# Kernel tuning notes

Measured on AMD Instinct MI355X. Metric: run time of the kernel, lower is better.

## Reference

```python
import jax, jax.numpy as jnp
import numpy as np

H = 16           # num_heads
D = 1024         # hidden_size
HD = D // H      # head_dim = 64
LN_EPS = 1e-5


def setup_inputs() -> dict:
    key = jax.random.key(0)
    ks = jax.random.split(key, 11)
    s = 1.0 / np.sqrt(D)
    x = jax.random.normal(ks[0], (2, 2048, D), dtype=jnp.float32)
    Wq = jax.random.uniform(ks[1], (D, D), jnp.float32, -s, s)
    bq = jax.random.uniform(ks[2], (D,), jnp.float32, -s, s)
    Wk = jax.random.uniform(ks[3], (D, D), jnp.float32, -s, s)
    bk = jax.random.uniform(ks[4], (D,), jnp.float32, -s, s)
    Wv = jax.random.uniform(ks[5], (D, D), jnp.float32, -s, s)
    bv = jax.random.uniform(ks[6], (D,), jnp.float32, -s, s)
    Wo = jax.random.uniform(ks[7], (D, D), jnp.float32, -s, s)
    bo = jax.random.uniform(ks[8], (D,), jnp.float32, -s, s)
    gamma = jnp.ones((D,), jnp.float32)
    beta = jnp.zeros((D,), jnp.float32)
    return {"x": x, "Wq": Wq, "bq": bq, "Wk": Wk, "bk": bk,
            "Wv": Wv, "bv": bv, "Wo": Wo, "bo": bo,
            "gamma": gamma, "beta": beta}


def reference(x, Wq, bq, Wk, bk, Wv, bv, Wo, bo, gamma, beta):
    B, S, _ = x.shape
    # projections -> [B, H, S, HD]
    def split_heads(t):
        return t.reshape(B, S, H, HD).transpose(0, 2, 1, 3)
    Q = split_heads(x @ Wq + bq)
    K = split_heads(x @ Wk + bk)
    V = split_heads(x @ Wv + bv)
    # scores [B, H, S, S], softmax over keys (dropout = identity in eval)
    scores = jnp.einsum('bhqd,bhkd->bhqk', Q, K) / np.sqrt(HD).astype(np.float32)
    attn = jax.nn.softmax(scores, axis=-1)
    ctx = jnp.einsum('bhqk,bhkd->bhqd', attn, V)          # [B, H, S, HD]
    ctx = ctx.transpose(0, 2, 1, 3).reshape(B, S, H * HD)  # [B, S, D]
    out = ctx @ Wo + bo
    # residual + LayerNorm
    y = out + x
    mu = jnp.mean(y, axis=-1, keepdims=True)
    var = jnp.mean(jnp.square(y - mu), axis=-1, keepdims=True)
    return (y - mu) * jax.lax.rsqrt(var + LN_EPS) * gamma + beta
```

## Files before the change

kernel.cpp:

```cpp
#include <hip/hip_runtime.h>
#include <cstdint>
#include <cstddef>


typedef short  b16x8  __attribute__((ext_vector_type(8)));
typedef float  f32x4  __attribute__((ext_vector_type(4)));
typedef float  f32x16 __attribute__((ext_vector_type(16)));

#define AS1 __attribute__((address_space(1)))
#define AS3 __attribute__((address_space(3)))

__device__ __forceinline__ unsigned short f2bf(float f) {
    unsigned int u = __builtin_bit_cast(unsigned int, f);
    u += 0x7FFFu + ((u >> 16) & 1u);
    return (unsigned short)(u >> 16);
}

__device__ __forceinline__ unsigned int cvt_pk_bf16(float lo, float hi) {
    unsigned int r;
    asm("v_cvt_pk_bf16_f32 %0, %1, %2" : "=v"(r) : "v"(lo), "v"(hi));
    return r;
}

__device__ __forceinline__ float exp2_fast(float x) {
    float r;
    asm("v_exp_f32 %0, %1" : "=v"(r) : "v"(x));
    return r;
}

__device__ __forceinline__ void permswap(unsigned &a, unsigned &b) {
    asm volatile("v_permlane32_swap_b32 %0, %1" : "+v"(a), "+v"(b));
}

__global__ __launch_bounds__(256) void k_cvt_x(const float* __restrict__ x,
                                               unsigned short* __restrict__ xb) {
    int i = blockIdx.x * 256 + threadIdx.x;
    size_t base = (size_t)i * 8;
    float4 v0 = *(const float4*)(x + base);
    float4 v1 = *(const float4*)(x + base + 4);
    int row = (int)(base >> 10), col = (int)(base & 1023);
    int rt = row >> 7, rr = row & 127, kt = col >> 6, cc = col & 63;
    int e = (rr * 64 + cc) ^ ((rr & 7) << 3);
    unsigned short o[8];
    o[0] = f2bf(v0.x); o[1] = f2bf(v0.y); o[2] = f2bf(v0.z); o[3] = f2bf(v0.w);
    o[4] = f2bf(v1.x); o[5] = f2bf(v1.y); o[6] = f2bf(v1.z); o[7] = f2bf(v1.w);
    *(uint4*)(xb + (size_t)(rt * 16 + kt) * 8192 + e) = *(uint4*)o;
}

__global__ __launch_bounds__(1024) void k_cvt_w(
    const float* __restrict__ W0, const float* __restrict__ W1,
    const float* __restrict__ W2, const float* __restrict__ W3,
    unsigned short* __restrict__ T0, unsigned short* __restrict__ T1,
    unsigned short* __restrict__ T2, unsigned short* __restrict__ T3) {
    const float* W = blockIdx.z == 0 ? W0 : blockIdx.z == 1 ? W1 : blockIdx.z == 2 ? W2 : W3;
    unsigned short* T = blockIdx.z == 0 ? T0 : blockIdx.z == 1 ? T1 : blockIdx.z == 2 ? T2 : T3;
    __shared__ float tile[32][33];
    int k0 = blockIdx.x * 32, n0 = blockIdx.y * 32;
    int tx = threadIdx.x, ty = threadIdx.y;
    tile[ty][tx] = W[(size_t)(k0 + ty) * 1024 + n0 + tx];
    __syncthreads();
    int n = n0 + ty, k = k0 + tx;
    unsigned short v = f2bf(tile[tx][ty]);
    if (blockIdx.z == 3) {
        T[(size_t)n * 1024 + k] = v;
    } else {
        int r = n & 127, c = k & 63;
        int e = (r * 64 + c) ^ ((r & 7) << 3);
        T[(size_t)((n >> 7) * 16 + (k >> 6)) * 8192 + e] = v;
    }
}

__global__ __launch_bounds__(512) void k_gemm_qkv(
    const unsigned short* __restrict__ A, const unsigned short* __restrict__ Bt,
    const float* __restrict__ bq, const float* __restrict__ bk, const float* __restrict__ bv,
    unsigned short* __restrict__ Qb, unsigned short* __restrict__ Kt,
    unsigned short* __restrict__ Vt) {
    __shared__ unsigned short As[2][8192];
    __shared__ unsigned short Bs[2][8192];
    const int tid = threadIdx.x, lane = tid & 63, wid = tid >> 6;
    const int m0 = blockIdx.y * 128, n0 = blockIdx.x * 128;
    const int wr = wid >> 2, wc = wid & 3;
    const int g = lane >> 4, r = lane & 15;
    f32x4 acc[4][2] = {};

    const unsigned short* Abase = A  + (size_t)blockIdx.y * 16 * 8192;
    const unsigned short* Bbase = Bt + (size_t)blockIdx.x * 16 * 8192;

#define GSTAGE(kt, buf) do {                                                              \
        const unsigned short* _a = Abase + (size_t)(kt) * 8192 + tid * 8;                 \
        const unsigned short* _b = Bbase + (size_t)(kt) * 8192 + tid * 8;                 \
        __builtin_amdgcn_global_load_lds((const AS1 void*)(_a),        (AS3 void*)((char*)As[buf] + tid * 16),        16, 0, 0); \
        __builtin_amdgcn_global_load_lds((const AS1 void*)(_a + 4096), (AS3 void*)((char*)As[buf] + 8192 + tid * 16), 16, 0, 0); \
        __builtin_amdgcn_global_load_lds((const AS1 void*)(_b),        (AS3 void*)((char*)Bs[buf] + tid * 16),        16, 0, 0); \
        __builtin_amdgcn_global_load_lds((const AS1 void*)(_b + 4096), (AS3 void*)((char*)Bs[buf] + 8192 + tid * 16), 16, 0, 0); \
    } while (0)

    GSTAGE(0, 0);
    __syncthreads();

    for (int kt = 0; kt < 16; ++kt) {
        const int cur = kt & 1;
        const unsigned short* Ac = As[cur];
        const unsigned short* Bc = Bs[cur];
        if (kt < 15) GSTAGE(kt + 1, cur ^ 1);
#pragma unroll
        for (int kk = 0; kk < 2; ++kk) {
            b16x8 af[4], bfr[2];
#pragma unroll
            for (int mi = 0; mi < 4; ++mi) {
                int row = wr * 64 + mi * 16 + r;
                int e = (row * 64 + kk * 32 + g * 8) ^ ((row & 7) << 3);
                af[mi] = __builtin_bit_cast(b16x8, *(const uint4*)(Ac + e));
            }
#pragma unroll
            for (int ni = 0; ni < 2; ++ni) {
                int row = wc * 32 + ni * 16 + r;
                int e = (row * 64 + kk * 32 + g * 8) ^ ((row & 7) << 3);
                bfr[ni] = __builtin_bit_cast(b16x8, *(const uint4*)(Bc + e));
            }
#pragma unroll
            for (int mi = 0; mi < 4; ++mi)
#pragma unroll
                for (int ni = 0; ni < 2; ++ni)
                    acc[mi][ni] = __builtin_amdgcn_mfma_f32_16x16x32_bf16(af[mi], bfr[ni], acc[mi][ni], 0, 0, 0);
        }
        __syncthreads();
    }
#undef GSTAGE

    for (int ni = 0; ni < 2; ++ni) {
        int col = n0 + wc * 32 + ni * 16 + r;
        int which = col >> 10, c = col & 1023;
        const float* bp = which == 0 ? bq : which == 1 ? bk : bv;
        float bvv = bp[c];
        int h = c >> 6, hd = c & 63;
        for (int mi = 0; mi < 4; ++mi)
            for (int j = 0; j < 4; ++j) {
                int row = m0 + wr * 64 + mi * 16 + g * 4 + j;
                float v = acc[mi][ni][j] + bvv;
                int b = row >> 11, s = row & 2047;
                size_t bh = (size_t)(b * 16 + h);
                if (which == 0) {
                    Qb[(bh * 2048 + s) * 64 + hd] = f2bf(v * 0.180336881f);
                } else if (which == 1) {
                    int tt = s >> 6, kr = s & 63;
                    Kt[(bh * 32 + tt) * 4096 + ((kr * 64 + hd) ^ ((kr & 7) << 3))] = f2bf(v);
                } else {
                    int tt = s >> 6, cc = s & 63;
                    Vt[(bh * 32 + tt) * 4096 + ((hd * 64 + cc) ^ ((hd & 7) << 3))] = f2bf(v);
                }
            }
    }
}

__global__ __launch_bounds__(512) void k_gemm_proj(
    const unsigned short* __restrict__ A, const unsigned short* __restrict__ Bt,
    const float* __restrict__ bias, float* __restrict__ out) {
    __shared__ unsigned short As[2][128 * 32];
    __shared__ unsigned short Bs[2][64 * 32];
    const int tid = threadIdx.x, lane = tid & 63, wid = tid >> 6;
    const int m0 = blockIdx.y * 128, n0 = blockIdx.x * 64;
    const int wr = wid >> 1, wc = wid & 1;
    f32x4 acc[2][2] = {};

    const int srow = tid >> 2, scol = (tid & 3) * 8;
    const unsigned short* Ag = A  + (size_t)(m0 + srow) * 1024 + scol;
    const unsigned short* Bg = Bt + (size_t)(n0 + srow) * 1024 + scol;

#define PSTAGE(kt, buf) do {                                                              \
        __builtin_amdgcn_global_load_lds((const AS1 void*)(Ag + (kt) * 32),               \
                                         (AS3 void*)((char*)As[buf] + tid * 16), 16, 0, 0); \
        if (tid < 256)                                                                    \
            __builtin_amdgcn_global_load_lds((const AS1 void*)(Bg + (kt) * 32),           \
                                             (AS3 void*)((char*)Bs[buf] + tid * 16), 16, 0, 0); \
    } while (0)

    PSTAGE(0, 0);
    __syncthreads();

    const int g = lane >> 4, r = lane & 15;
    for (int kt = 0; kt < 32; ++kt) {
        const int cur = kt & 1;
        if (kt < 31) PSTAGE(kt + 1, cur ^ 1);
        b16x8 af[2], bfr[2];
#pragma unroll
        for (int mi = 0; mi < 2; ++mi)
            af[mi] = __builtin_bit_cast(b16x8, *(const uint4*)(As[cur] + (wr * 32 + mi * 16 + r) * 32 + g * 8));
#pragma unroll
        for (int ni = 0; ni < 2; ++ni)
            bfr[ni] = __builtin_bit_cast(b16x8, *(const uint4*)(Bs[cur] + (wc * 32 + ni * 16 + r) * 32 + g * 8));
#pragma unroll
        for (int mi = 0; mi < 2; ++mi)
#pragma unroll
            for (int ni = 0; ni < 2; ++ni)
                acc[mi][ni] = __builtin_amdgcn_mfma_f32_16x16x32_bf16(af[mi], bfr[ni], acc[mi][ni], 0, 0, 0);
        __syncthreads();
    }
#undef PSTAGE

    for (int mi = 0; mi < 2; ++mi)
        for (int ni = 0; ni < 2; ++ni) {
            int col = n0 + wc * 32 + ni * 16 + r;
            float bv = bias[col];
            for (int j = 0; j < 4; ++j) {
                int row = m0 + wr * 32 + mi * 16 + g * 4 + j;
                out[(size_t)row * 1024 + col] = acc[mi][ni][j] + bv;
            }
        }
}

#define TSWZ(row, byteoff) ((((row) * 128) + (byteoff)) ^ (((row) & 7) << 4))

__global__ __launch_bounds__(512, 4) void k_attn(const unsigned short* __restrict__ Qb,
                                                 const unsigned short* __restrict__ Kt,
                                                 const unsigned short* __restrict__ Vt,
                                                 unsigned short* __restrict__ ctx) {
    __shared__ unsigned short Ks[2][2][4096];
    __shared__ unsigned short Vs[2][2][4096];
    __shared__ float lsh[4][64];
    const int tid = threadIdx.x, lane = tid & 63, w = tid >> 6;
    const int q32 = lane & 31, hi = lane >> 5;
    const int wq = w & 3, grp = w >> 2;
    const int lt = wq * 64 + lane;

    int bid = blockIdx.x;
    int xcd = bid & 7, idx = bid >> 3;
    int bh = xcd * 4 + (idx & 3);
    int q0 = (idx >> 2) * 128;
    const int b = bh >> 4, h = bh & 15;

    const unsigned short* qrow = Qb + ((size_t)bh * 2048 + q0 + wq * 32 + q32) * 64 + hi * 8;
    b16x8 qf[4];
#pragma unroll
    for (int ds = 0; ds < 4; ++ds)
        qf[ds] = __builtin_bit_cast(b16x8, *(const uint4*)(qrow + ds * 16));

    const unsigned short* Kg = Kt + (size_t)bh * 32 * 4096;
    const unsigned short* Vg = Vt + (size_t)bh * 32 * 4096;
    const int ktbase = grp * 16;

#define STAGE(i, buf) do {                                                                \
        const unsigned short* _ks = Kg + (size_t)(ktbase + (i)) * 4096 + lt * 8;          \
        const unsigned short* _vs = Vg + (size_t)(ktbase + (i)) * 4096 + lt * 8;          \
        __builtin_amdgcn_global_load_lds((const AS1 void*)_ks,          (AS3 void*)((char*)Ks[grp][buf] + lt * 16),        16, 0, 0); \
        __builtin_amdgcn_global_load_lds((const AS1 void*)(_ks + 2048), (AS3 void*)((char*)Ks[grp][buf] + 4096 + lt * 16), 16, 0, 0); \
        __builtin_amdgcn_global_load_lds((const AS1 void*)_vs,          (AS3 void*)((char*)Vs[grp][buf] + lt * 16),        16, 0, 0); \
        __builtin_amdgcn_global_load_lds((const AS1 void*)(_vs + 2048), (AS3 void*)((char*)Vs[grp][buf] + 4096 + lt * 16), 16, 0, 0); \
    } while (0)

    float lpart = 0.f;
    f32x16 oacc[2] = {};

    STAGE(0, 0);
    __syncthreads();

    for (int i = 0; i < 16; ++i) {
        const int cur = i & 1;
        if (i < 15) STAGE(i + 1, cur ^ 1);

        f32x16 sacc[2] = {};
        __builtin_amdgcn_s_setprio(1);
#pragma unroll
        for (int ds = 0; ds < 4; ++ds) {
            b16x8 kf0 = __builtin_bit_cast(b16x8, *(const uint4*)((char*)Ks[grp][cur] + TSWZ(q32,      ds * 32 + hi * 16)));
            b16x8 kf1 = __builtin_bit_cast(b16x8, *(const uint4*)((char*)Ks[grp][cur] + TSWZ(32 + q32, ds * 32 + hi * 16)));
            sacc[0] = __builtin_amdgcn_mfma_f32_32x32x16_bf16(kf0, qf[ds], sacc[0], 0, 0, 0);
            sacc[1] = __builtin_amdgcn_mfma_f32_32x32x16_bf16(kf1, qf[ds], sacc[1], 0, 0, 0);
        }
        __builtin_amdgcn_s_setprio(0);

        float pb[2][16];
#pragma unroll
        for (int kb = 0; kb < 2; ++kb)
#pragma unroll
            for (int reg = 0; reg < 16; ++reg)
                pb[kb][reg] = exp2_fast(sacc[kb][reg]);
        {
            float t0 = (pb[0][0]  + pb[0][1])  + (pb[0][2]  + pb[0][3]);
            float t1 = (pb[0][4]  + pb[0][5])  + (pb[0][6]  + pb[0][7]);
            float t2 = (pb[0][8]  + pb[0][9])  + (pb[0][10] + pb[0][11]);
            float t3 = (pb[0][12] + pb[0][13]) + (pb[0][14] + pb[0][15]);
            float t4 = (pb[1][0]  + pb[1][1])  + (pb[1][2]  + pb[1][3]);
            float t5 = (pb[1][4]  + pb[1][5])  + (pb[1][6]  + pb[1][7]);
            float t6 = (pb[1][8]  + pb[1][9])  + (pb[1][10] + pb[1][11]);
            float t7 = (pb[1][12] + pb[1][13]) + (pb[1][14] + pb[1][15]);
            lpart += ((t0 + t1) + (t2 + t3)) + ((t4 + t5) + (t6 + t7));
        }
        unsigned wv[2][4][2];
#pragma unroll
        for (int kb = 0; kb < 2; ++kb)
#pragma unroll
            for (int rg = 0; rg < 4; ++rg) {
                wv[kb][rg][0] = cvt_pk_bf16(pb[kb][rg * 4 + 0], pb[kb][rg * 4 + 1]);
                wv[kb][rg][1] = cvt_pk_bf16(pb[kb][rg * 4 + 2], pb[kb][rg * 4 + 3]);
            }
        b16x8 pa[4];
#pragma unroll
        for (int ks = 0; ks < 4; ++ks) {
            int kb = ks >> 1, rg0 = (ks & 1) * 2;
            unsigned u0 = wv[kb][rg0][0], u2 = wv[kb][rg0 + 1][0];
            permswap(u0, u2);
            unsigned u1 = wv[kb][rg0][1], u3 = wv[kb][rg0 + 1][1];
            permswap(u1, u3);
            uint4 uu; uu.x = u0; uu.y = u1; uu.z = u2; uu.w = u3;
            pa[ks] = __builtin_bit_cast(b16x8, uu);
        }
        __builtin_amdgcn_s_setprio(1);
#pragma unroll
        for (int ks = 0; ks < 4; ++ks) {
            b16x8 vf0 = __builtin_bit_cast(b16x8, *(const uint4*)((char*)Vs[grp][cur] + TSWZ(q32,      ks * 32 + hi * 16)));
            b16x8 vf1 = __builtin_bit_cast(b16x8, *(const uint4*)((char*)Vs[grp][cur] + TSWZ(32 + q32, ks * 32 + hi * 16)));
            oacc[0] = __builtin_amdgcn_mfma_f32_32x32x16_bf16(pa[ks], vf0, oacc[0], 0, 0, 0);
            oacc[1] = __builtin_amdgcn_mfma_f32_32x32x16_bf16(pa[ks], vf1, oacc[1], 0, 0, 0);
        }
        __builtin_amdgcn_s_setprio(0);
        __syncthreads();
    }

    {
        unsigned a = __builtin_bit_cast(unsigned, lpart), bb = a;
        permswap(a, bb);
        lpart = __builtin_bit_cast(float, a) + __builtin_bit_cast(float, bb);
    }

    float* s0 = (float*)Ks[1];
    float* s1 = (float*)Vs[1];
    if (grp == 1) {
        int base = (wq * 64 + lane) * 16;
#pragma unroll
        for (int reg = 0; reg < 16; ++reg) {
            s0[base + reg] = oacc[0][reg];
            s1[base + reg] = oacc[1][reg];
        }
        lsh[wq][lane] = lpart;
    }
    __syncthreads();
    if (grp == 0) {
        float l = lpart + lsh[wq][lane];
        float inv = 1.f / l;
        int base = (wq * 64 + lane) * 16;
#pragma unroll
        for (int reg = 0; reg < 16; ++reg) {
            int qr = (reg & 3) + 8 * (reg >> 2) + 4 * hi;
            float iv = __shfl(inv, qr, 64);
            float o0 = (oacc[0][reg] + s0[base + reg]) * iv;
            float o1 = (oacc[1][reg] + s1[base + reg]) * iv;
            unsigned short* dst = ctx + ((size_t)(b * 2048 + q0 + wq * 32 + qr)) * 1024 + h * 64 + q32;
            dst[0]  = f2bf(o0);
            dst[32] = f2bf(o1);
        }
    }
#undef STAGE
}

__global__ __launch_bounds__(256) void k_ln(const float* __restrict__ proj,
                                            const float* __restrict__ x,
                                            const float* __restrict__ gamma,
                                            const float* __restrict__ beta,
                                            float* __restrict__ out) {
    int t = threadIdx.x, lane = t & 63, w = t >> 6;
    int row = blockIdx.x * 4 + w;
    const float4* pr = (const float4*)(proj + (size_t)row * 1024);
    const float4* xr = (const float4*)(x    + (size_t)row * 1024);
    float4 y[4];
    float s = 0.f, ss = 0.f;
#pragma unroll
    for (int i = 0; i < 4; ++i) {
        float4 a = pr[lane + i * 64], bx = xr[lane + i * 64];
        float4 yy;
        yy.x = a.x + bx.x; yy.y = a.y + bx.y; yy.z = a.z + bx.z; yy.w = a.w + bx.w;
        y[i] = yy;
        s  += yy.x + yy.y + yy.z + yy.w;
        ss += yy.x * yy.x + yy.y * yy.y + yy.z * yy.z + yy.w * yy.w;
    }
#pragma unroll
    for (int o = 32; o > 0; o >>= 1) {
        s  += __shfl_xor(s,  o, 64);
        ss += __shfl_xor(ss, o, 64);
    }
    float mu  = s * (1.f / 1024.f);
    float var = ss * (1.f / 1024.f) - mu * mu;
    float inv = rsqrtf(var + 1e-5f);
    float4* outr = (float4*)(out + (size_t)row * 1024);
    const float4* gr = (const float4*)gamma;
    const float4* br = (const float4*)beta;
#pragma unroll
    for (int i = 0; i < 4; ++i) {
        float4 g4 = gr[lane + i * 64], b4 = br[lane + i * 64];
        float4 o4;
        o4.x = (y[i].x - mu) * inv * g4.x + b4.x;
        o4.y = (y[i].y - mu) * inv * g4.y + b4.y;
        o4.z = (y[i].z - mu) * inv * g4.z + b4.z;
        o4.w = (y[i].w - mu) * inv * g4.w + b4.w;
        outr[lane + i * 64] = o4;
    }
}

extern "C" void kernel_launch(void* const* d_in, const int* in_sizes, int n_in,
                              void* d_out, int out_size, void* d_ws, size_t ws_size,
                              hipStream_t stream) {
    const float* x  = (const float*)d_in[0];
    const float* Wq = (const float*)d_in[1];
    const float* bq = (const float*)d_in[2];
    const float* Wk = (const float*)d_in[3];
    const float* bk = (const float*)d_in[4];
    const float* Wv = (const float*)d_in[5];
    const float* bv = (const float*)d_in[6];
    const float* Wo = (const float*)d_in[7];
    const float* bo = (const float*)d_in[8];
    const float* gamma = (const float*)d_in[9];
    const float* beta  = (const float*)d_in[10];

    char* ws = (char*)d_ws;
    const size_t MB = 1u << 20;
    unsigned short* xbf   = (unsigned short*)(ws);
    unsigned short* Wqkvt = (unsigned short*)(ws + 8 * MB);
    unsigned short* Wot   = (unsigned short*)(ws + 14 * MB);
    unsigned short* Qb    = (unsigned short*)(ws + 16 * MB);
    unsigned short* Kt    = (unsigned short*)(ws + 24 * MB);
    unsigned short* Vt    = (unsigned short*)(ws + 32 * MB);
    float* proj = (float*)(ws + 16 * MB);
    unsigned short* ctx = xbf;

    k_cvt_x<<<2048, 256, 0, stream>>>(x, xbf);
    k_cvt_w<<<dim3(32, 32, 4), dim3(32, 32), 0, stream>>>(
        Wq, Wk, Wv, Wo, Wqkvt, Wqkvt + 1024 * 1024, Wqkvt + 2 * 1024 * 1024, Wot);
    k_gemm_qkv<<<dim3(24, 32), 512, 0, stream>>>(xbf, Wqkvt, bq, bk, bv, Qb, Kt, Vt);
    k_attn<<<512, 512, 0, stream>>>(Qb, Kt, Vt, ctx);
    k_gemm_proj<<<dim3(16, 32), 512, 0, stream>>>(ctx, Wot, bo, proj);
    k_ln<<<1024, 256, 0, stream>>>(proj, x, gamma, beta, (float*)d_out);
}
```

Before: 130.3 us.

## Restructure QKV GEMM into 256x256 tiles with phased prefetch and XCD remap

The QKV projection GEMM moves from 128x128 tiles to 256x256 tiles per 512-thread block. Operands are re-laid out by the conversion kernels into 64-row swizzled sub-tiles and loaded in four phases, with partial vmcnt waits so that loading the next k-step overlaps MFMA work. The 1D grid is remapped so neighbouring tiles land on the same XCD. The goal is more data reuse per LDS byte and less exposed load latency, at the cost of only 192 blocks, which may leave some CUs idle. Separately, the s_setprio hints around the attention MFMA loops are removed.

```diff
diff --git a/kernel.cpp b/kernel.cpp
--- a/kernel.cpp
+++ b/kernel.cpp
@@ -39,12 +39,12 @@
     float4 v0 = *(const float4*)(x + base);
     float4 v1 = *(const float4*)(x + base + 4);
     int row = (int)(base >> 10), col = (int)(base & 1023);
-    int rt = row >> 7, rr = row & 127, kt = col >> 6, cc = col & 63;
+    int qi = row >> 6, rr = row & 63, kt = col >> 6, cc = col & 63;
     int e = (rr * 64 + cc) ^ ((rr & 7) << 3);
     unsigned short o[8];
     o[0] = f2bf(v0.x); o[1] = f2bf(v0.y); o[2] = f2bf(v0.z); o[3] = f2bf(v0.w);
     o[4] = f2bf(v1.x); o[5] = f2bf(v1.y); o[6] = f2bf(v1.z); o[7] = f2bf(v1.w);
-    *(uint4*)(xb + (size_t)(rt * 16 + kt) * 8192 + e) = *(uint4*)o;
+    *(uint4*)(xb + (size_t)(qi * 16 + kt) * 4096 + e) = *(uint4*)o;
 }
 
 __global__ __launch_bounds__(1024) void k_cvt_w(
@@ -64,9 +64,9 @@
     if (blockIdx.z == 3) {
         T[(size_t)n * 1024 + k] = v;
     } else {
-        int r = n & 127, c = k & 63;
-        int e = (r * 64 + c) ^ ((r & 7) << 3);
-        T[(size_t)((n >> 7) * 16 + (k >> 6)) * 8192 + e] = v;
+        int rr = n & 63, cc = k & 63;
+        int e = (rr * 64 + cc) ^ ((rr & 7) << 3);
+        T[(size_t)((n >> 6) * 16 + (k >> 6)) * 4096 + e] = v;
     }
 }
 
@@ -75,69 +75,102 @@
     const float* __restrict__ bq, const float* __restrict__ bk, const float* __restrict__ bv,
     unsigned short* __restrict__ Qb, unsigned short* __restrict__ Kt,
     unsigned short* __restrict__ Vt) {
-    __shared__ unsigned short As[2][8192];
-    __shared__ unsigned short Bs[2][8192];
+    __shared__ unsigned short As[2][4][4096];
+    __shared__ unsigned short Bs[2][4][4096];
     const int tid = threadIdx.x, lane = tid & 63, wid = tid >> 6;
-    const int m0 = blockIdx.y * 128, n0 = blockIdx.x * 128;
     const int wr = wid >> 2, wc = wid & 3;
     const int g = lane >> 4, r = lane & 15;
-    f32x4 acc[4][2] = {};
-
-    const unsigned short* Abase = A  + (size_t)blockIdx.y * 16 * 8192;
-    const unsigned short* Bbase = Bt + (size_t)blockIdx.x * 16 * 8192;
-
-#define GSTAGE(kt, buf) do {                                                              \
-        const unsigned short* _a = Abase + (size_t)(kt) * 8192 + tid * 8;                 \
-        const unsigned short* _b = Bbase + (size_t)(kt) * 8192 + tid * 8;                 \
-        __builtin_amdgcn_global_load_lds((const AS1 void*)(_a),        (AS3 void*)((char*)As[buf] + tid * 16),        16, 0, 0); \
-        __builtin_amdgcn_global_load_lds((const AS1 void*)(_a + 4096), (AS3 void*)((char*)As[buf] + 8192 + tid * 16), 16, 0, 0); \
-        __builtin_amdgcn_global_load_lds((const AS1 void*)(_b),        (AS3 void*)((char*)Bs[buf] + tid * 16),        16, 0, 0); \
-        __builtin_amdgcn_global_load_lds((const AS1 void*)(_b + 4096), (AS3 void*)((char*)Bs[buf] + 8192 + tid * 16), 16, 0, 0); \
-    } while (0)
-
-    GSTAGE(0, 0);
-    __syncthreads();
+
+    int bid = blockIdx.x;
+    int wg = (bid & 7) * 24 + (bid >> 3);
+    int bx = wg % 12, by = wg / 12;
+
+    f32x4 acc[8][4] = {};
+    b16x8 bfr[4][2];
+
+    const unsigned short* Ab = A  + (size_t)(by * 4) * 16 * 4096;
+    const unsigned short* Bb = Bt + (size_t)(bx * 4) * 16 * 4096;
+
+#define SA(kt_, q_, d_) __builtin_amdgcn_global_load_lds(                                  \
+        (const AS1 void*)(Ab + ((size_t)(q_) * 16 + (kt_)) * 4096 + tid * 8),              \
+        (AS3 void*)((char*)As[d_][q_] + tid * 16), 16, 0, 0)
+#define SB(kt_, q_, d_) __builtin_amdgcn_global_load_lds(                                  \
+        (const AS1 void*)(Bb + ((size_t)(q_) * 16 + (kt_)) * 4096 + tid * 8),              \
+        (AS3 void*)((char*)Bs[d_][q_] + tid * 16), 16, 0, 0)
+
+#define LD8(base_, row_, kk_) __builtin_bit_cast(b16x8, *(const uint4*)(                   \
+        (const char*)(base_) + (row_) * 128 + ((((kk_) * 64) + g * 16) ^ (((row_) & 7) << 4))))
+
+#define MFMA16(a_, b_, c_) __builtin_amdgcn_mfma_f32_16x16x32_bf16(a_, b_, c_, 0, 0, 0)
+
+    SA(0, 0, 0); SA(0, 1, 0); SA(0, 2, 0); SA(0, 3, 0);
+    SB(0, 0, 0); SB(0, 1, 0); SB(0, 2, 0); SB(0, 3, 0);
+    SA(1, 0, 1); SA(1, 1, 1);
+
+#define DO_PHASE(p, STAGES)                                                                \
+    {                                                                                      \
+        STAGES                                                                             \
+        if ((p) == 0) {                                                                    \
+            if (kt < 15) asm volatile("s_waitcnt vmcnt(6)" ::: "memory");                  \
+            else         asm volatile("s_waitcnt vmcnt(0)" ::: "memory");                  \
+        }                                                                                  \
+        __builtin_amdgcn_s_barrier();                                                      \
+        __builtin_amdgcn_sched_barrier(0);                                                 \
+        const char* _aq = (const char*)As[d][wr * 2 + ((p) >> 1)];                         \
+        const int _row0 = ((2 * (p)) & 3) * 16 + r;                                        \
+        const int _row1 = ((2 * (p) + 1) & 3) * 16 + r;                                    \
+        b16x8 a0k0 = LD8(_aq, _row0, 0), a0k1 = LD8(_aq, _row0, 1);                        \
+        b16x8 a1k0 = LD8(_aq, _row1, 0), a1k1 = LD8(_aq, _row1, 1);                        \
+        if ((p) == 0) {                                                                    \
+            const char* _bq = (const char*)Bs[d][wc];                                      \
+            _Pragma("unroll")                                                              \
+            for (int ni = 0; ni < 4; ++ni) {                                               \
+                int rowb = ni * 16 + r;                                                    \
+                bfr[ni][0] = LD8(_bq, rowb, 0);                                            \
+                bfr[ni][1] = LD8(_bq, rowb, 1);                                            \
+            }                                                                              \
+        }                                                                                  \
+        __builtin_amdgcn_s_setprio(1);                                                     \
+        _Pragma("unroll")                                                                  \
+        for (int ni = 0; ni < 4; ++ni) {                                                   \
+            acc[2 * (p)][ni]     = MFMA16(a0k0, bfr[ni][0], acc[2 * (p)][ni]);             \
+            acc[2 * (p)][ni]     = MFMA16(a0k1, bfr[ni][1], acc[2 * (p)][ni]);             \
+            acc[2 * (p) + 1][ni] = MFMA16(a1k0, bfr[ni][0], acc[2 * (p) + 1][ni]);         \
+            acc[2 * (p) + 1][ni] = MFMA16(a1k1, bfr[ni][1], acc[2 * (p) + 1][ni]);         \
+        }                                                                                  \
+        __builtin_amdgcn_s_setprio(0);                                                     \
+        __builtin_amdgcn_s_barrier();                                                      \
+        __builtin_amdgcn_sched_barrier(0);                                                 \
+    }
 
     for (int kt = 0; kt < 16; ++kt) {
-        const int cur = kt & 1;
-        const unsigned short* Ac = As[cur];
-        const unsigned short* Bc = Bs[cur];
-        if (kt < 15) GSTAGE(kt + 1, cur ^ 1);
-#pragma unroll
-        for (int kk = 0; kk < 2; ++kk) {
-            b16x8 af[4], bfr[2];
-#pragma unroll
-            for (int mi = 0; mi < 4; ++mi) {
-                int row = wr * 64 + mi * 16 + r;
-                int e = (row * 64 + kk * 32 + g * 8) ^ ((row & 7) << 3);
-                af[mi] = __builtin_bit_cast(b16x8, *(const uint4*)(Ac + e));
-            }
-#pragma unroll
-            for (int ni = 0; ni < 2; ++ni) {
-                int row = wc * 32 + ni * 16 + r;
-                int e = (row * 64 + kk * 32 + g * 8) ^ ((row & 7) << 3);
-                bfr[ni] = __builtin_bit_cast(b16x8, *(const uint4*)(Bc + e));
-            }
-#pragma unroll
-            for (int mi = 0; mi < 4; ++mi)
-#pragma unroll
-                for (int ni = 0; ni < 2; ++ni)
-                    acc[mi][ni] = __builtin_amdgcn_mfma_f32_16x16x32_bf16(af[mi], bfr[ni], acc[mi][ni], 0, 0, 0);
-        }
-        __syncthreads();
-    }
-#undef GSTAGE
-
-    for (int ni = 0; ni < 2; ++ni) {
-        int col = n0 + wc * 32 + ni * 16 + r;
+        const int d = kt & 1;
+        DO_PHASE(0,
+            if (kt < 15) { SA(kt + 1, 2, d ^ 1); SA(kt + 1, 3, d ^ 1);
+                           SB(kt + 1, 0, d ^ 1); SB(kt + 1, 1, d ^ 1); })
+        DO_PHASE(1,
+            if (kt < 15) { SB(kt + 1, 2, d ^ 1); SB(kt + 1, 3, d ^ 1); })
+        DO_PHASE(2,
+            if (kt < 14) { SA(kt + 2, 0, d); SA(kt + 2, 1, d); })
+        DO_PHASE(3, )
+    }
+#undef DO_PHASE
+#undef SA
+#undef SB
+#undef LD8
+#undef MFMA16
+
+    const int m0 = by * 256, n0 = bx * 256;
+    for (int ni = 0; ni < 4; ++ni) {
+        int col = n0 + wc * 64 + ni * 16 + r;
         int which = col >> 10, c = col & 1023;
         const float* bp = which == 0 ? bq : which == 1 ? bk : bv;
         float bvv = bp[c];
         int h = c >> 6, hd = c & 63;
-        for (int mi = 0; mi < 4; ++mi)
+        for (int mf = 0; mf < 8; ++mf)
             for (int j = 0; j < 4; ++j) {
-                int row = m0 + wr * 64 + mi * 16 + g * 4 + j;
-                float v = acc[mi][ni][j] + bvv;
+                int row = m0 + wr * 128 + mf * 16 + g * 4 + j;
+                float v = acc[mf][ni][j] + bvv;
                 int b = row >> 11, s = row & 2047;
                 size_t bh = (size_t)(b * 16 + h);
                 if (which == 0) {
@@ -259,7 +292,6 @@
         if (i < 15) STAGE(i + 1, cur ^ 1);
 
         f32x16 sacc[2] = {};
-        __builtin_amdgcn_s_setprio(1);
 #pragma unroll
         for (int ds = 0; ds < 4; ++ds) {
             b16x8 kf0 = __builtin_bit_cast(b16x8, *(const uint4*)((char*)Ks[grp][cur] + TSWZ(q32,      ds * 32 + hi * 16)));
@@ -267,7 +299,6 @@
             sacc[0] = __builtin_amdgcn_mfma_f32_32x32x16_bf16(kf0, qf[ds], sacc[0], 0, 0, 0);
             sacc[1] = __builtin_amdgcn_mfma_f32_32x32x16_bf16(kf1, qf[ds], sacc[1], 0, 0, 0);
         }
-        __builtin_amdgcn_s_setprio(0);
 
         float pb[2][16];
 #pragma unroll
@@ -305,7 +336,6 @@
             uint4 uu; uu.x = u0; uu.y = u1; uu.z = u2; uu.w = u3;
             pa[ks] = __builtin_bit_cast(b16x8, uu);
         }
-        __builtin_amdgcn_s_setprio(1);
 #pragma unroll
         for (int ks = 0; ks < 4; ++ks) {
             b16x8 vf0 = __builtin_bit_cast(b16x8, *(const uint4*)((char*)Vs[grp][cur] + TSWZ(q32,      ks * 32 + hi * 16)));
@@ -313,7 +343,6 @@
             oacc[0] = __builtin_amdgcn_mfma_f32_32x32x16_bf16(pa[ks], vf0, oacc[0], 0, 0, 0);
             oacc[1] = __builtin_amdgcn_mfma_f32_32x32x16_bf16(pa[ks], vf1, oacc[1], 0, 0, 0);
         }
-        __builtin_amdgcn_s_setprio(0);
         __syncthreads();
     }
 
@@ -425,7 +454,7 @@
     k_cvt_x<<<2048, 256, 0, stream>>>(x, xbf);
     k_cvt_w<<<dim3(32, 32, 4), dim3(32, 32), 0, stream>>>(
         Wq, Wk, Wv, Wo, Wqkvt, Wqkvt + 1024 * 1024, Wqkvt + 2 * 1024 * 1024, Wot);
-    k_gemm_qkv<<<dim3(24, 32), 512, 0, stream>>>(xbf, Wqkvt, bq, bk, bv, Qb, Kt, Vt);
+    k_gemm_qkv<<<192, 512, 0, stream>>>(xbf, Wqkvt, bq, bk, bv, Qb, Kt, Vt);
     k_attn<<<512, 512, 0, stream>>>(Qb, Kt, Vt, ctx);
     k_gemm_proj<<<dim3(16, 32), 512, 0, stream>>>(ctx, Wot, bo, proj);
     k_ln<<<1024, 256, 0, stream>>>(proj, x, gamma, beta, (float*)d_out);
```

Result: slower. 169.9 us (+30.4%).
